# Optimization experiments

Measured on AMD Instinct MI355X. Metric: run time of the kernel, lower is better.

The kernel has to match this reference:

```python
import jax, jax.numpy as jnp
import numpy as np

SLOPE = (1.0 / 8 + 1.0 / 3) / 2  # F.rrelu in eval mode: mean of (lower, upper)
DILS = [1, 2, 4, 8, 16]
WINDOW = 32
TEMP = 0.1


def rrelu(x):
    return jnp.where(x >= 0, x, x * SLOPE)


def conv1d(x, w, b, dil):
    # x: [B, Cin, T], w: [Cout, Cin, K]
    y = jax.lax.conv_general_dilated(x, w, window_strides=(1,), padding='VALID',
                                     rhs_dilation=(dil,),
                                     dimension_numbers=('NCH', 'OIH', 'NCH'))
    return y + b[None, :, None]


def setup_inputs() -> dict:
    key = jax.random.key(0)
    ks = jax.random.split(key, 32)
    B, T, R, K, W = 16, 16384, 8, 2, WINDOW
    ins = [1, 64, 64, 64, 64]
    outs = [64, 64, 64, 64, R]
    inp = {"x": jax.random.normal(ks[0], (B, 1, T), jnp.float32)}
    for l in range(5):
        inp[f"cw{l}"] = jax.random.normal(ks[1 + l], (outs[l], ins[l], K), jnp.float32) * 0.1
        inp[f"cb{l}"] = jax.random.normal(ks[6 + l], (outs[l],), jnp.float32) * 0.1
    pc = [(2 * R, 2 * R), (2 * R, 2 * R), (1, 2 * R)]  # params_convs, kernel 1
    for i, (o, ci) in enumerate(pc):
        inp[f"mw{i}"] = jax.random.normal(ks[11 + i], (o, ci, 1), jnp.float32) * 0.1
        inp[f"mb{i}"] = jax.random.normal(ks[14 + i], (o,), jnp.float32) * 0.1
    inp["sqrt_cov_tt"] = jax.random.uniform(ks[17], (R, 1), jnp.float32)
    inp["fish_jt"] = jax.random.normal(ks[18], (R, W), jnp.float32) * 0.01
    u = jax.random.uniform(ks[19], (B, T, R), jnp.float32, minval=1e-6, maxval=1.0 - 1e-6)
    inp["gumbel"] = -jnp.log(-jnp.log(u))
    return inp


def reference(x, cw0, cb0, cw1, cb1, cw2, cb2, cw3, cb3, cw4, cb4,
              mw0, mb0, mw1, mb1, mw2, mb2, sqrt_cov_tt, fish_jt, gumbel):
    pad = sum(DILS)
    T = x.shape[-1]
    W = WINDOW
    # forward_pass: causal dilated conv stack with rrelu
    h = jnp.pad(x, ((0, 0), (0, 0), (pad, 0)))
    for w, b, d in zip([cw0, cw1, cw2, cw3, cw4], [cb0, cb1, cb2, cb3, cb4], DILS):
        h = rrelu(conv1d(h, w, b, d))
    # h: [B, R, T]
    logits = jnp.transpose(h, (0, 2, 1))  # [B, T, R]
    gen_z = jax.nn.softmax((logits + gumbel) / TEMP, axis=-1)
    gen_z = jnp.transpose(gen_z, (0, 2, 1))  # [B, R, T]
    # params_convs (1x1 convs): conv -> (rrelu, conv) x2
    m = conv1d(jnp.concatenate([gen_z, h], axis=1), mw0, mb0, 1)
    m = conv1d(rrelu(m), mw1, mb1, 1)
    mus = conv1d(rrelu(m), mw2, mb2, 1)  # [B, 1, T]
    cov_tt = jnp.einsum('brt,rl->blt', gen_z, sqrt_cov_tt) ** 2  # [B, 1, T]
    cov_tt = cov_tt[:, :, W:T]  # [B, 1, T-W]
    fj = jnp.einsum('brt,rw->bwt', gen_z, fish_jt)[:, :, W:T]  # [B, W, T-W]
    # vectorized sliding window: x_window[b, j, t] = x[b, 0, t + j]
    idx = jnp.arange(W)[:, None] + jnp.arange(T - W)[None, :]  # [W, T-W]
    xw = x[:, 0, :][:, idx]   # [B, W, T-W]
    mw_ = mus[:, 0, :][:, idx]  # [B, W, T-W]
    _mus = mus[:, 0, W:T] - jnp.einsum('bwt,bwt->bt', cov_tt * fj, xw - mw_)
    return (_mus, gen_z)
```

## Files before the change

### kernel.cpp

```cpp
#include <hip/hip_runtime.h>
#include <hip/hip_bf16.h>

#define NT 512
#define TT 192
#define PBA 222
#define PBB 220
#define NB 16
#define T_ 16384
#define W_ 32
#define TW_ (T_ - W_)
#define SLOPE_C 0.22916666666666666f

typedef short v8s __attribute__((ext_vector_type(8)));
typedef float v4f __attribute__((ext_vector_type(4)));

__device__ __forceinline__ float rr(float v){ return v >= 0.f ? v : v * SLOPE_C; }
__device__ __forceinline__ ushort f2bs(float f){ __hip_bfloat16 h = __float2bfloat16(f); return *(ushort*)&h; }
__device__ __forceinline__ float bs2f(ushort u){ union{unsigned i; float f;} v; v.i = ((unsigned)u) << 16; return v.f; }

__device__ __forceinline__ int agr(int p, int gi){ return p*128 + ((gi ^ (p & 15)) << 3); }
__device__ __forceinline__ int widx(int wr, int ci){
  return wr*64 + ((((ci >> 3) ^ (wr & 7)) << 3) | (ci & 7));
}

__device__ __forceinline__ void scatter_w(const float4 w[4], ushort* wlds, int tid){
#pragma unroll
  for (int j = 0; j < 4; ++j){
    const float* e = (const float*)&w[j];
#pragma unroll
    for (int q = 0; q < 4; ++q){
      int l = (tid + j*NT)*4 + q;
      int c = l >> 7, rem = l & 127, ci = rem >> 1, k = rem & 1;
      float v = e[q];
      ushort h = f2bs(v);
      ushort lo = f2bs(v - bs2f(h));
      int wr = k*64 + c;
      int ix = widx(wr, ci);
      wlds[ix] = h;
      wlds[8192 + ix] = lo;
    }
  }
}

template<int D, int NSRC, int NDST>
__device__ __forceinline__ void mfma_layer(const ushort* __restrict__ src,
    ushort* __restrict__ dst, const ushort* __restrict__ wlds,
    const float* __restrict__ cbias, int tid)
{
  const int wave = tid >> 6;
  if (wave >= 7) return;
  const int lane = tid & 63;
  const int n = lane & 15, quad = lane >> 4;
  const int p0 = wave * 32;

  v4f acc[8];
  const v4f vz = {0.f, 0.f, 0.f, 0.f};
#pragma unroll
  for (int i = 0; i < 8; ++i) acc[i] = vz;

#pragma unroll
  for (int tap = 0; tap < 2; ++tap){
#pragma unroll
    for (int kb = 0; kb < 2; ++kb){
      const int kg = kb*4 + quad;
      v8s wh[4], wl[4], ah[2], al[2];
#pragma unroll
      for (int mt = 0; mt < 4; ++mt){
        int wr = tap*64 + mt*16 + n;
        int base = wr*64 + ((kg ^ (wr & 7)) << 3);
        wh[mt] = *(const v8s*)(wlds + base);
        wl[mt] = *(const v8s*)(wlds + 8192 + base);
      }
#pragma unroll
      for (int nt = 0; nt < 2; ++nt){
        int p = p0 + nt*16 + n + tap*D;
        if (p >= NSRC) p = NSRC - 1;
        ah[nt] = *(const v8s*)(src + agr(p, kg));
        al[nt] = *(const v8s*)(src + agr(p, 8 + kg));
      }
#pragma unroll
      for (int nt = 0; nt < 2; ++nt)
#pragma unroll
        for (int mt = 0; mt < 4; ++mt){
          v4f a = acc[nt*4 + mt];
          a = __builtin_amdgcn_mfma_f32_16x16x32_bf16(wh[mt], ah[nt], a, 0, 0, 0);
          a = __builtin_amdgcn_mfma_f32_16x16x32_bf16(wh[mt], al[nt], a, 0, 0, 0);
          a = __builtin_amdgcn_mfma_f32_16x16x32_bf16(wl[mt], ah[nt], a, 0, 0, 0);
          acc[nt*4 + mt] = a;
        }
    }
  }

#pragma unroll
  for (int nt = 0; nt < 2; ++nt){
    int p = p0 + nt*16 + n;
    if (p < NDST){
#pragma unroll
      for (int mt = 0; mt < 4; ++mt){
#pragma unroll
        for (int r = 0; r < 4; r += 2){
          int c = mt*16 + quad*4 + r;
          float y0 = rr(acc[nt*4 + mt][r]     + cbias[c]);
          float y1 = rr(acc[nt*4 + mt][r + 1] + cbias[c + 1]);
          ushort h0 = f2bs(y0), h1 = f2bs(y1);
          ushort l0 = f2bs(y0 - bs2f(h0)), l1 = f2bs(y1 - bs2f(h1));
          int gh = agr(p, c >> 3)       + (c & 7);
          int gl = agr(p, 8 + (c >> 3)) + (c & 7);
          *(unsigned*)(dst + gh) = (unsigned)h0 | ((unsigned)h1 << 16);
          *(unsigned*)(dst + gl) = (unsigned)l0 | ((unsigned)l1 << 16);
        }
      }
    }
  }
}

template<bool GZT>
__global__ __launch_bounds__(NT) void kA(
    const float* __restrict__ x,
    const float* __restrict__ cw0, const float* __restrict__ cb0,
    const float* __restrict__ cw1, const float* __restrict__ cb1,
    const float* __restrict__ cw2, const float* __restrict__ cb2,
    const float* __restrict__ cw3, const float* __restrict__ cb3,
    const float* __restrict__ cw4, const float* __restrict__ cb4,
    const float* __restrict__ mw0, const float* __restrict__ mb0,
    const float* __restrict__ mw1, const float* __restrict__ mb1,
    const float* __restrict__ mw2, const float* __restrict__ mb2,
    const float* __restrict__ gum,
    float* __restrict__ ws_mus, float* __restrict__ out_gz,
    float* __restrict__ gzt)
{
  __shared__ ushort bufA[PBA*128];
  __shared__ ushort bufB[PBB*128];
  __shared__ ushort wlds[20480 + 1600];

  ushort* wlds4 = wlds + 16384;
  float*  cst   = (float*)(wlds + 20480);
  float*  xbuf  = (float*)bufB;

  const int tile = blockIdx.x, b = blockIdx.y;
  const int t0 = tile * TT;
  const int core = (T_ - t0 < TT) ? (T_ - t0) : TT;
  const int tid = threadIdx.x;

  float4 wpre[4];
  { const float4* g = (const float4*)cw1;
    wpre[0] = g[tid]; wpre[1] = g[tid + NT];
    wpre[2] = g[tid + 2*NT]; wpre[3] = g[tid + 3*NT]; }

  const int nx = core + 31;
  for (int i = tid; i < nx; i += NT){
    int g = t0 + i;
    xbuf[i] = (g >= 31) ? x[(size_t)b*T_ + g - 31] : 0.f;
  }
  for (int l = tid; l < 1024; l += NT){
    int c = l >> 7, rem = l & 127, ci = rem >> 1, k = rem & 1;
    float v = cw4[l];
    ushort h = f2bs(v); ushort lo = f2bs(v - bs2f(h));
    int ix = widx(k*16 + c, ci);
    wlds4[ix] = h;
    wlds4[2048 + ix] = lo;
  }
  for (int z = tid; z < 2048; z += NT){
    int pl = z >> 10, rem = z & 1023, k = rem >> 9, rem2 = rem & 511;
    int m = 8 + (rem2 >> 6), ci = rem2 & 63;
    wlds4[pl*2048 + widx(k*16 + m, ci)] = 0;
  }
  for (int i = tid; i < 256; i += NT){ cst[i] = mw0[i]; cst[256 + i] = mw1[i]; }
  if (tid < 16){ cst[512+tid] = mw2[tid]; cst[528+tid] = mb0[tid]; cst[544+tid] = mb1[tid]; }
  if (tid == 0) cst[560] = mb2[0];
  if (tid < 8)   cst[576+tid] = cb4[tid];
  if (tid < 128) cst[592+tid] = cw0[tid];
  if (tid < 64)  cst[720+tid] = cb0[tid];
  __syncthreads();

  scatter_w(wpre, wlds, tid);
  { const float4* g = (const float4*)cw2;
    wpre[0] = g[tid]; wpre[1] = g[tid + NT];
    wpre[2] = g[tid + 2*NT]; wpre[3] = g[tid + 3*NT]; }
  {
    const int n0 = core + 30;
    for (int i = tid; i < PBA*64; i += NT){
      int p = i >> 6, c = i & 63;
      float y = 0.f;
      if (p < n0) y = rr(cst[720 + c] + cst[592 + 2*c]*xbuf[p] + cst[593 + 2*c]*xbuf[p + 1]);
      ushort h = f2bs(y); ushort lo = f2bs(y - bs2f(h));
      bufA[agr(p, c >> 3)       + (c & 7)] = h;
      bufA[agr(p, 8 + (c >> 3)) + (c & 7)] = lo;
    }
  }
  __syncthreads();

  mfma_layer<2, PBA, PBB>(bufA, bufB, wlds, cb1, tid);
  __syncthreads();
  scatter_w(wpre, wlds, tid);
  { const float4* g = (const float4*)cw3;
    wpre[0] = g[tid]; wpre[1] = g[tid + NT];
    wpre[2] = g[tid + 2*NT]; wpre[3] = g[tid + 3*NT]; }
  __syncthreads();
  mfma_layer<4, PBB, PBA>(bufB, bufA, wlds, cb2, tid);
  __syncthreads();
  scatter_w(wpre, wlds, tid);
  __syncthreads();
  mfma_layer<8, PBA, PBB>(bufA, bufB, wlds, cb3, tid);
  __syncthreads();

  float* h4s = (float*)bufA;
  {
    const int wave = tid >> 6;
    if (wave < 7){
      const int lane = tid & 63;
      const int n = lane & 15, quad = lane >> 4;
      const int p0 = wave * 32;
      v4f acc2[2];
      const v4f vz = {0.f, 0.f, 0.f, 0.f};
      acc2[0] = vz; acc2[1] = vz;
#pragma unroll
      for (int tap = 0; tap < 2; ++tap){
#pragma unroll
        for (int kb = 0; kb < 2; ++kb){
          const int kg = kb*4 + quad;
          int wr = tap*16 + n;
          int base = wr*64 + ((kg ^ (wr & 7)) << 3);
          v8s wh = *(const v8s*)(wlds4 + base);
          v8s wl = *(const v8s*)(wlds4 + 2048 + base);
#pragma unroll
          for (int nt = 0; nt < 2; ++nt){
            int p = p0 + nt*16 + n + tap*16;
            if (p >= PBB) p = PBB - 1;
            v8s ah = *(const v8s*)(bufB + agr(p, kg));
            v8s al = *(const v8s*)(bufB + agr(p, 8 + kg));
            v4f a = acc2[nt];
            a = __builtin_amdgcn_mfma_f32_16x16x32_bf16(wh, ah, a, 0, 0, 0);
            a = __builtin_amdgcn_mfma_f32_16x16x32_bf16(wh, al, a, 0, 0, 0);
            a = __builtin_amdgcn_mfma_f32_16x16x32_bf16(wl, ah, a, 0, 0, 0);
            acc2[nt] = a;
          }
        }
      }
#pragma unroll
      for (int nt = 0; nt < 2; ++nt){
        int p = p0 + nt*16 + n;
        if (p < core && quad < 2){
#pragma unroll
          for (int r = 0; r < 4; ++r){
            int c = quad*4 + r;
            h4s[c*TT + p] = rr(acc2[nt][r] + cst[576 + c]);
          }
        }
      }
    }
  }
  __syncthreads();

  if (tid < core){
    const int t = t0 + tid;
    float l[8];
#pragma unroll
    for (int r = 0; r < 8; ++r) l[r] = h4s[r*TT + tid];
    float gv[8];
    *(float4*)&gv[0] = *(const float4*)(gum + (size_t)(b*T_ + t)*8);
    *(float4*)&gv[4] = *(const float4*)(gum + (size_t)(b*T_ + t)*8 + 4);
    float s[8], mx = -1e30f;
#pragma unroll
    for (int r = 0; r < 8; ++r){ s[r] = (l[r] + gv[r]) * 10.0f; mx = fmaxf(mx, s[r]); }
    float e[8], sum = 0.f;
#pragma unroll
    for (int r = 0; r < 8; ++r){ e[r] = __expf(s[r] - mx); sum += e[r]; }
    float inv = 1.0f / sum;
    float z[8];
#pragma unroll
    for (int r = 0; r < 8; ++r){
      z[r] = e[r] * inv;
      out_gz[(size_t)(b*8 + r)*T_ + t] = z[r];
    }
    if (GZT){
      *(float4*)(gzt + (size_t)(b*T_ + t)*8)     = make_float4(z[0], z[1], z[2], z[3]);
      *(float4*)(gzt + (size_t)(b*T_ + t)*8 + 4) = make_float4(z[4], z[5], z[6], z[7]);
    }
    float m0[16];
#pragma unroll
    for (int o = 0; o < 16; ++o){
      float a = cst[528 + o];
#pragma unroll
      for (int i = 0; i < 8; ++i) a += cst[o*16 + i] * z[i];
#pragma unroll
      for (int i = 0; i < 8; ++i) a += cst[o*16 + 8 + i] * l[i];
      m0[o] = rr(a);
    }
    float m1[16];
#pragma unroll
    for (int o = 0; o < 16; ++o){
      float a = cst[544 + o];
#pragma unroll
      for (int i = 0; i < 16; ++i) a += cst[256 + o*16 + i] * m0[i];
      m1[o] = rr(a);
    }
    float mu = cst[560];
#pragma unroll
    for (int i = 0; i < 16; ++i) mu += cst[512 + i] * m1[i];
    ws_mus[(size_t)b*T_ + t] = mu;
  }
}

template<bool GZT>
__global__ __launch_bounds__(256) void kB(
    const float* __restrict__ x, const float* __restrict__ fish,
    const float* __restrict__ sct, const float* __restrict__ ws_mus,
    const float* __restrict__ gz, float* __restrict__ out0)
{
  __shared__ float xm[288], mm[288], fs[256], sc[8];
  const int b = blockIdx.y;
  const int s = blockIdx.x * 256;
  const int tid = threadIdx.x;
  for (int i = tid; i < 288; i += 256){
    int g = s + i;
    bool ok = g < T_;
    xm[i] = ok ? x[(size_t)b*T_ + g] : 0.f;
    mm[i] = ok ? ws_mus[(size_t)b*T_ + g] : 0.f;
  }
  fs[tid] = fish[tid];
  if (tid < 8) sc[tid] = sct[tid];
  __syncthreads();
  const int tp = s + tid;
  if (tp < TW_){
    const int t = W_ + tp;
    float z[8];
    if (GZT){
      *(float4*)&z[0] = *(const float4*)(gz + (size_t)(b*T_ + t)*8);
      *(float4*)&z[4] = *(const float4*)(gz + (size_t)(b*T_ + t)*8 + 4);
    } else {
#pragma unroll
      for (int r = 0; r < 8; ++r) z[r] = gz[(size_t)(b*8 + r)*T_ + t];
    }
    float cv = 0.f;
#pragma unroll
    for (int r = 0; r < 8; ++r) cv += sc[r] * z[r];
    cv *= cv;
    float acc = 0.f;
#pragma unroll 4
    for (int w = 0; w < 32; ++w){
      float fj = 0.f;
#pragma unroll
      for (int r = 0; r < 8; ++r) fj += z[r] * fs[r*32 + w];
      acc += fj * (xm[tid + w] - mm[tid + w]);
    }
    out0[(size_t)b*TW_ + tp] = mm[tid + 32] - cv * acc;
  }
}

extern "C" void kernel_launch(void* const* d_in, const int* in_sizes, int n_in,
                              void* d_out, int out_size, void* d_ws, size_t ws_size,
                              hipStream_t stream)
{
  const float* x   = (const float*)d_in[0];
  const float* cw0 = (const float*)d_in[1];
  const float* cb0 = (const float*)d_in[2];
  const float* cw1 = (const float*)d_in[3];
  const float* cb1 = (const float*)d_in[4];
  const float* cw2 = (const float*)d_in[5];
  const float* cb2 = (const float*)d_in[6];
  const float* cw3 = (const float*)d_in[7];
  const float* cb3 = (const float*)d_in[8];
  const float* cw4 = (const float*)d_in[9];
  const float* cb4 = (const float*)d_in[10];
  const float* mw0 = (const float*)d_in[11];
  const float* mb0 = (const float*)d_in[12];
  const float* mw1 = (const float*)d_in[13];
  const float* mb1 = (const float*)d_in[14];
  const float* mw2 = (const float*)d_in[15];
  const float* mb2 = (const float*)d_in[16];
  const float* sct = (const float*)d_in[17];
  const float* fish= (const float*)d_in[18];
  const float* gum = (const float*)d_in[19];

  float* out0   = (float*)d_out;
  float* out_gz = out0 + NB*TW_;
  float* ws_mus = (float*)d_ws;
  float* gzt    = ws_mus + (size_t)NB*T_;

  const bool use_t = ws_size >= (size_t)NB*T_*9*sizeof(float);

  dim3 gA((T_ + TT - 1) / TT, NB);
  dim3 gB((TW_ + 255) / 256, NB);
  if (use_t){
    kA<true><<<gA, NT, 0, stream>>>(x, cw0, cb0, cw1, cb1, cw2, cb2, cw3, cb3, cw4, cb4,
                                    mw0, mb0, mw1, mb1, mw2, mb2, gum, ws_mus, out_gz, gzt);
    kB<true><<<gB, 256, 0, stream>>>(x, fish, sct, ws_mus, gzt, out0);
  } else {
    kA<false><<<gA, NT, 0, stream>>>(x, cw0, cb0, cw1, cb1, cw2, cb2, cw3, cb3, cw4, cb4,
                                     mw0, mb0, mw1, mb1, mw2, mb2, gum, ws_mus, out_gz, gzt);
    kB<false><<<gB, 256, 0, stream>>>(x, fish, sct, ws_mus, out_gz, out0);
  }
}
```

Before: 230.1 us.

## Precompute bf16 split weight images in a prep kernel and double block size

```diff
diff --git a/kernel.cpp b/kernel.cpp
--- a/kernel.cpp
+++ b/kernel.cpp
@@ -1,7 +1,7 @@
 #include <hip/hip_runtime.h>
 #include <hip/hip_bf16.h>
 
-#define NT 512
+#define NT 1024
 #define TT 192
 #define PBA 222
 #define PBB 220
@@ -11,6 +11,10 @@
 #define TW_ (T_ - W_)
 #define SLOPE_C 0.22916666666666666f
 
+#define WIMG_W4   49152
+#define WIMG_CST  53248
+#define WIMG_USH  55296
+
 typedef short v8s __attribute__((ext_vector_type(8)));
 typedef float v4f __attribute__((ext_vector_type(4)));
 
@@ -23,22 +27,56 @@
   return wr*64 + ((((ci >> 3) ^ (wr & 7)) << 3) | (ci & 7));
 }
 
-__device__ __forceinline__ void scatter_w(const float4 w[4], ushort* wlds, int tid){
-#pragma unroll
-  for (int j = 0; j < 4; ++j){
-    const float* e = (const float*)&w[j];
-#pragma unroll
-    for (int q = 0; q < 4; ++q){
-      int l = (tid + j*NT)*4 + q;
-      int c = l >> 7, rem = l & 127, ci = rem >> 1, k = rem & 1;
-      float v = e[q];
-      ushort h = f2bs(v);
-      ushort lo = f2bs(v - bs2f(h));
-      int wr = k*64 + c;
-      int ix = widx(wr, ci);
-      wlds[ix] = h;
-      wlds[8192 + ix] = lo;
-    }
+__global__ __launch_bounds__(256) void kW(
+    const float* __restrict__ cw1, const float* __restrict__ cw2,
+    const float* __restrict__ cw3, const float* __restrict__ cw4,
+    const float* __restrict__ cw0, const float* __restrict__ cb0,
+    const float* __restrict__ cb1, const float* __restrict__ cb2,
+    const float* __restrict__ cb3, const float* __restrict__ cb4,
+    const float* __restrict__ mw0, const float* __restrict__ mb0,
+    const float* __restrict__ mw1, const float* __restrict__ mb1,
+    const float* __restrict__ mw2, const float* __restrict__ mb2,
+    ushort* __restrict__ wimg)
+{
+  const int id = blockIdx.x*256 + threadIdx.x;
+  if (id < 24576){
+    int l = id >> 13, e = id & 8191;
+    const float* src = (l == 0) ? cw1 : ((l == 1) ? cw2 : cw3);
+    int c = e >> 7, rem = e & 127, ci = rem >> 1, k = rem & 1;
+    float v = src[e];
+    ushort h = f2bs(v), lo = f2bs(v - bs2f(h));
+    int ix = widx(k*64 + c, ci);
+    wimg[l*16384 + ix] = h;
+    wimg[l*16384 + 8192 + ix] = lo;
+  } else if (id < 25600){
+    int e = id - 24576;
+    int c = e >> 7, rem = e & 127, ci = rem >> 1, k = rem & 1;
+    float v = cw4[e];
+    ushort h = f2bs(v), lo = f2bs(v - bs2f(h));
+    int ix = widx(k*16 + c, ci);
+    wimg[WIMG_W4 + ix] = h;
+    wimg[WIMG_W4 + 2048 + ix] = lo;
+  } else if (id < 27648){
+    int e = id - 25600;
+    int pl = e >> 10, rem = e & 1023, k = rem >> 9, r2 = rem & 511;
+    int m = 8 + (r2 >> 6), ci = r2 & 63;
+    wimg[WIMG_W4 + pl*2048 + widx(k*16 + m, ci)] = 0;
+  } else if (id < 28672){
+    int e = id - 27648;
+    float v = 0.f;
+    if      (e < 256) v = mw0[e];
+    else if (e < 512) v = mw1[e - 256];
+    else if (e < 528) v = mw2[e - 512];
+    else if (e < 544) v = mb0[e - 528];
+    else if (e < 560) v = mb1[e - 544];
+    else if (e < 561) v = mb2[0];
+    else if (e >= 576 && e < 584) v = cb4[e - 576];
+    else if (e >= 592 && e < 720) v = cw0[e - 592];
+    else if (e >= 720 && e < 784) v = cb0[e - 720];
+    else if (e >= 784 && e < 848) v = cb1[e - 784];
+    else if (e >= 848 && e < 912) v = cb2[e - 848];
+    else if (e >= 912 && e < 976) v = cb3[e - 912];
+    ((float*)(wimg + WIMG_CST))[e] = v;
   }
 }
 
@@ -115,74 +153,44 @@
 }
 
 template<bool GZT>
-__global__ __launch_bounds__(NT) void kA(
-    const float* __restrict__ x,
-    const float* __restrict__ cw0, const float* __restrict__ cb0,
-    const float* __restrict__ cw1, const float* __restrict__ cb1,
-    const float* __restrict__ cw2, const float* __restrict__ cb2,
-    const float* __restrict__ cw3, const float* __restrict__ cb3,
-    const float* __restrict__ cw4, const float* __restrict__ cb4,
-    const float* __restrict__ mw0, const float* __restrict__ mb0,
-    const float* __restrict__ mw1, const float* __restrict__ mb1,
-    const float* __restrict__ mw2, const float* __restrict__ mb2,
-    const float* __restrict__ gum,
+__global__ __launch_bounds__(NT, 4) void kA(
+    const float* __restrict__ x, const float* __restrict__ gum,
+    const ushort* __restrict__ wimg,
     float* __restrict__ ws_mus, float* __restrict__ out_gz,
     float* __restrict__ gzt)
 {
-  __shared__ ushort bufA[PBA*128];
-  __shared__ ushort bufB[PBB*128];
-  __shared__ ushort wlds[20480 + 1600];
-
-  ushort* wlds4 = wlds + 16384;
-  float*  cst   = (float*)(wlds + 20480);
-  float*  xbuf  = (float*)bufB;
+  __shared__ __align__(16) ushort bufA[PBA*128];
+  __shared__ __align__(16) ushort bufB[PBB*128];
+  __shared__ __align__(16) ushort wlds[16384];
+  __shared__ __align__(16) ushort w4lds[4096];
+  __shared__ __align__(16) float  cstl[1024];
+
+  float* xbuf = (float*)bufB;
 
   const int tile = blockIdx.x, b = blockIdx.y;
   const int t0 = tile * TT;
   const int core = (T_ - t0 < TT) ? (T_ - t0) : TT;
   const int tid = threadIdx.x;
 
-  float4 wpre[4];
-  { const float4* g = (const float4*)cw1;
-    wpre[0] = g[tid]; wpre[1] = g[tid + NT];
-    wpre[2] = g[tid + 2*NT]; wpre[3] = g[tid + 3*NT]; }
-
   const int nx = core + 31;
   for (int i = tid; i < nx; i += NT){
     int g = t0 + i;
     xbuf[i] = (g >= 31) ? x[(size_t)b*T_ + g - 31] : 0.f;
   }
-  for (int l = tid; l < 1024; l += NT){
-    int c = l >> 7, rem = l & 127, ci = rem >> 1, k = rem & 1;
-    float v = cw4[l];
-    ushort h = f2bs(v); ushort lo = f2bs(v - bs2f(h));
-    int ix = widx(k*16 + c, ci);
-    wlds4[ix] = h;
-    wlds4[2048 + ix] = lo;
-  }
-  for (int z = tid; z < 2048; z += NT){
-    int pl = z >> 10, rem = z & 1023, k = rem >> 9, rem2 = rem & 511;
-    int m = 8 + (rem2 >> 6), ci = rem2 & 63;
-    wlds4[pl*2048 + widx(k*16 + m, ci)] = 0;
-  }
-  for (int i = tid; i < 256; i += NT){ cst[i] = mw0[i]; cst[256 + i] = mw1[i]; }
-  if (tid < 16){ cst[512+tid] = mw2[tid]; cst[528+tid] = mb0[tid]; cst[544+tid] = mb1[tid]; }
-  if (tid == 0) cst[560] = mb2[0];
-  if (tid < 8)   cst[576+tid] = cb4[tid];
-  if (tid < 128) cst[592+tid] = cw0[tid];
-  if (tid < 64)  cst[720+tid] = cb0[tid];
-  __syncthreads();
-
-  scatter_w(wpre, wlds, tid);
-  { const float4* g = (const float4*)cw2;
-    wpre[0] = g[tid]; wpre[1] = g[tid + NT];
-    wpre[2] = g[tid + 2*NT]; wpre[3] = g[tid + 3*NT]; }
+  for (int i = tid; i < 2048; i += NT)
+    *(v8s*)(wlds + i*8) = *(const v8s*)(wimg + i*8);
+  for (int i = tid; i < 512; i += NT)
+    *(v8s*)(w4lds + i*8) = *(const v8s*)(wimg + WIMG_W4 + i*8);
+  for (int i = tid; i < 512; i += NT)
+    ((float2*)cstl)[i] = ((const float2*)(wimg + WIMG_CST))[i];
+  __syncthreads();
+
   {
     const int n0 = core + 30;
     for (int i = tid; i < PBA*64; i += NT){
       int p = i >> 6, c = i & 63;
       float y = 0.f;
-      if (p < n0) y = rr(cst[720 + c] + cst[592 + 2*c]*xbuf[p] + cst[593 + 2*c]*xbuf[p + 1]);
+      if (p < n0) y = rr(cstl[720 + c] + cstl[592 + 2*c]*xbuf[p] + cstl[593 + 2*c]*xbuf[p + 1]);
       ushort h = f2bs(y); ushort lo = f2bs(y - bs2f(h));
       bufA[agr(p, c >> 3)       + (c & 7)] = h;
       bufA[agr(p, 8 + (c >> 3)) + (c & 7)] = lo;
@@ -190,18 +198,17 @@
   }
   __syncthreads();
 
-  mfma_layer<2, PBA, PBB>(bufA, bufB, wlds, cb1, tid);
-  __syncthreads();
-  scatter_w(wpre, wlds, tid);
-  { const float4* g = (const float4*)cw3;
-    wpre[0] = g[tid]; wpre[1] = g[tid + NT];
-    wpre[2] = g[tid + 2*NT]; wpre[3] = g[tid + 3*NT]; }
-  __syncthreads();
-  mfma_layer<4, PBB, PBA>(bufB, bufA, wlds, cb2, tid);
-  __syncthreads();
-  scatter_w(wpre, wlds, tid);
-  __syncthreads();
-  mfma_layer<8, PBA, PBB>(bufA, bufB, wlds, cb3, tid);
+  mfma_layer<2, PBA, PBB>(bufA, bufB, wlds, cstl + 784, tid);
+  __syncthreads();
+  for (int i = tid; i < 2048; i += NT)
+    *(v8s*)(wlds + i*8) = *(const v8s*)(wimg + 16384 + i*8);
+  __syncthreads();
+  mfma_layer<4, PBB, PBA>(bufB, bufA, wlds, cstl + 848, tid);
+  __syncthreads();
+  for (int i = tid; i < 2048; i += NT)
+    *(v8s*)(wlds + i*8) = *(const v8s*)(wimg + 32768 + i*8);
+  __syncthreads();
+  mfma_layer<8, PBA, PBB>(bufA, bufB, wlds, cstl + 912, tid);
   __syncthreads();
 
   float* h4s = (float*)bufA;
@@ -221,8 +228,8 @@
           const int kg = kb*4 + quad;
           int wr = tap*16 + n;
           int base = wr*64 + ((kg ^ (wr & 7)) << 3);
-          v8s wh = *(const v8s*)(wlds4 + base);
-          v8s wl = *(const v8s*)(wlds4 + 2048 + base);
+          v8s wh = *(const v8s*)(w4lds + base);
+          v8s wl = *(const v8s*)(w4lds + 2048 + base);
 #pragma unroll
           for (int nt = 0; nt < 2; ++nt){
             int p = p0 + nt*16 + n + tap*16;
@@ -244,7 +251,7 @@
 #pragma unroll
           for (int r = 0; r < 4; ++r){
             int c = quad*4 + r;
-            h4s[c*TT + p] = rr(acc2[nt][r] + cst[576 + c]);
+            h4s[c*TT + p] = rr(acc2[nt][r] + cstl[576 + c]);
           }
         }
       }
@@ -280,24 +287,24 @@
     float m0[16];
 #pragma unroll
     for (int o = 0; o < 16; ++o){
-      float a = cst[528 + o];
-#pragma unroll
-      for (int i = 0; i < 8; ++i) a += cst[o*16 + i] * z[i];
-#pragma unroll
-      for (int i = 0; i < 8; ++i) a += cst[o*16 + 8 + i] * l[i];
+      float a = cstl[528 + o];
+#pragma unroll
+      for (int i = 0; i < 8; ++i) a += cstl[o*16 + i] * z[i];
+#pragma unroll
+      for (int i = 0; i < 8; ++i) a += cstl[o*16 + 8 + i] * l[i];
       m0[o] = rr(a);
     }
     float m1[16];
 #pragma unroll
     for (int o = 0; o < 16; ++o){
-      float a = cst[544 + o];
-#pragma unroll
-      for (int i = 0; i < 16; ++i) a += cst[256 + o*16 + i] * m0[i];
+      float a = cstl[544 + o];
+#pragma unroll
+      for (int i = 0; i < 16; ++i) a += cstl[256 + o*16 + i] * m0[i];
       m1[o] = rr(a);
     }
-    float mu = cst[560];
-#pragma unroll
-    for (int i = 0; i < 16; ++i) mu += cst[512 + i] * m1[i];
+    float mu = cstl[560];
+#pragma unroll
+    for (int i = 0; i < 16; ++i) mu += cstl[512 + i] * m1[i];
     ws_mus[(size_t)b*T_ + t] = mu;
   }
 }
@@ -376,19 +383,22 @@
   float* out0   = (float*)d_out;
   float* out_gz = out0 + NB*TW_;
   float* ws_mus = (float*)d_ws;
-  float* gzt    = ws_mus + (size_t)NB*T_;
-
-  const bool use_t = ws_size >= (size_t)NB*T_*9*sizeof(float);
+  ushort* wimg  = (ushort*)(ws_mus + (size_t)NB*T_);
+  float* gzt    = ws_mus + (size_t)NB*T_ + WIMG_USH/2;
+
+  const size_t need_gzt = ((size_t)NB*T_ + WIMG_USH/2 + (size_t)8*NB*T_) * sizeof(float);
+  const bool use_t = ws_size >= need_gzt;
+
+  kW<<<112, 256, 0, stream>>>(cw1, cw2, cw3, cw4, cw0, cb0, cb1, cb2, cb3, cb4,
+                              mw0, mb0, mw1, mb1, mw2, mb2, wimg);
 
   dim3 gA((T_ + TT - 1) / TT, NB);
   dim3 gB((TW_ + 255) / 256, NB);
   if (use_t){
-    kA<true><<<gA, NT, 0, stream>>>(x, cw0, cb0, cw1, cb1, cw2, cb2, cw3, cb3, cw4, cb4,
-                                    mw0, mb0, mw1, mb1, mw2, mb2, gum, ws_mus, out_gz, gzt);
+    kA<true><<<gA, NT, 0, stream>>>(x, gum, wimg, ws_mus, out_gz, gzt);
     kB<true><<<gB, 256, 0, stream>>>(x, fish, sct, ws_mus, gzt, out0);
   } else {
-    kA<false><<<gA, NT, 0, stream>>>(x, cw0, cb0, cw1, cb1, cw2, cb2, cw3, cb3, cw4, cb4,
-                                     mw0, mb0, mw1, mb1, mw2, mb2, gum, ws_mus, out_gz, gzt);
+    kA<false><<<gA, NT, 0, stream>>>(x, gum, wimg, ws_mus, out_gz, gzt);
     kB<false><<<gB, 256, 0, stream>>>(x, fish, sct, ws_mus, out_gz, out0);
   }
 }
```

After: 231.3 us. Within noise of the previous version (+0.5%).
